# Kernel optimization log

Hardware: AMD Instinct MI355X
Metric: run time of the kernel (lower is better)

## Reference

```python
import jax, jax.numpy as jnp
import numpy as np

N = 100000          # nodes
E = 1600000         # edges (before self-loops)
F_IN = 256          # num_node_features
F_MID = F_IN // 2   # conv1 out = 128
HID = 128           # hidden_channels
OUT = 64            # num_label_features
G = 128             # num graphs in batch
NEG_SLOPE = 0.2


def setup_inputs() -> dict:
    key = jax.random.key(0)
    ks = jax.random.split(key, 16)
    s = 0.05
    return {
        "x": jax.random.normal(ks[0], (N, F_IN), dtype=jnp.float32),
        "edge_index": jax.random.randint(ks[1], (2, E), 0, N, dtype=jnp.int64),
        "batch": jnp.sort(jax.random.randint(ks[2], (N,), 0, G, dtype=jnp.int64)),
        # GATConv 1 (heads=1)
        "W1": jax.random.normal(ks[3], (F_IN, F_MID), jnp.float32) * s,
        "a1_src": jax.random.normal(ks[4], (F_MID,), jnp.float32) * s,
        "a1_dst": jax.random.normal(ks[5], (F_MID,), jnp.float32) * s,
        "b1": jnp.zeros((F_MID,), jnp.float32),
        # GATConv 2
        "W2": jax.random.normal(ks[6], (F_MID, HID), jnp.float32) * s,
        "a2_src": jax.random.normal(ks[7], (HID,), jnp.float32) * s,
        "a2_dst": jax.random.normal(ks[8], (HID,), jnp.float32) * s,
        "b2": jnp.zeros((HID,), jnp.float32),
        # GlobalAttention gate nn
        "gate_W": jax.random.normal(ks[9], (HID, 1), jnp.float32) * s,
        "gate_b": jnp.zeros((1,), jnp.float32),
        # final linear
        "lin_W": jax.random.normal(ks[10], (HID, OUT), jnp.float32) * s,
        "lin_b": jnp.zeros((OUT,), jnp.float32),
    }


def _gat_conv(x, edge_index, W, a_src, a_dst, bias):
    """PyG GATConv, heads=1, add_self_loops=True, negative_slope=0.2."""
    n = x.shape[0]
    h = x @ W                                   # [N, F]
    loop = jnp.arange(n, dtype=edge_index.dtype)
    src = jnp.concatenate([edge_index[0], loop])  # message sources j
    dst = jnp.concatenate([edge_index[1], loop])  # aggregation targets i
    # per-node attention logits, gathered per-edge
    al = (h @ a_src)[src] + (h @ a_dst)[dst]    # [E+N]
    al = jax.nn.leaky_relu(al, NEG_SLOPE)
    # segment softmax over incoming edges of each dst node
    m = jax.ops.segment_max(al, dst, num_segments=n)
    e = jnp.exp(al - m[dst])
    s = jax.ops.segment_sum(e, dst, num_segments=n)
    coef = e / (s[dst] + 1e-16)
    out = jax.ops.segment_sum(h[src] * coef[:, None], dst, num_segments=n)
    return out + bias


def reference(x, edge_index, batch, W1, a1_src, a1_dst, b1,
              W2, a2_src, a2_dst, b2, gate_W, gate_b, lin_W, lin_b):
    h = _gat_conv(x, edge_index, W1, a1_src, a1_dst, b1)
    h = jax.nn.relu(h)
    h = _gat_conv(h, edge_index, W2, a2_src, a2_dst, b2)
    # GlobalAttention pooling: segment softmax of gate over batch ids
    gate = (h @ gate_W + gate_b)[:, 0]          # [N]
    gm = jax.ops.segment_max(gate, batch, num_segments=G)
    ge = jnp.exp(gate - gm[batch])
    gs = jax.ops.segment_sum(ge, batch, num_segments=G)
    attn = ge / (gs[batch] + 1e-16)
    pooled = jax.ops.segment_sum(h * attn[:, None], batch, num_segments=G)  # [G, HID]
    pooled = jax.nn.relu(pooled)
    # dropout p=0.5 is identity at inference
    return pooled @ lin_W + lin_b               # [G, OUT]
```

## Files before the change

kernel.cpp:

```cpp
#include <hip/hip_runtime.h>
#include <hip/hip_bf16.h>
#include <math.h>

#define NNODES 100000
#define NEDGES 1600000
#define EN     1700000
#define F_IN   256
#define F_MID  128
#define HID    128
#define NG     128
#define NOUT   64
#define SCAN_CHUNK 2048
#define NCHUNK ((NNODES + SCAN_CHUNK - 1) / SCAN_CHUNK)

typedef unsigned int  u32;
typedef unsigned short u16;

__device__ __forceinline__ float bfl(u32 u) { return __uint_as_float(u << 16); }
__device__ __forceinline__ float bfh(u32 u) { return __uint_as_float(u & 0xFFFF0000u); }
__device__ __forceinline__ u32 f2bf(float f) {
    u32 x = __float_as_uint(f);
    return (x + 0x7FFFu + ((x >> 16) & 1u)) >> 16;
}

__global__ __launch_bounds__(256) void k_init(int* deg, float* gs, float* pooled) {
    int i = blockIdx.x * 256 + threadIdx.x;
    if (i < NNODES) deg[i] = 1;
    if (i < NG) gs[i] = 0.f;
    if (i < NG * HID) pooled[i] = 0.f;
}

__global__ __launch_bounds__(256) void k_count(const int* __restrict__ ei, int* deg) {
    int e = blockIdx.x * 256 + threadIdx.x;
    if (e >= NEDGES) return;
    atomicAdd(&deg[ei[NEDGES + e]], 1);
}

__global__ __launch_bounds__(256) void k_scan_chunk(const int* __restrict__ deg,
                                                    int* rowptr, int* part) {
    __shared__ int sums[256];
    int c = blockIdx.x, t = threadIdx.x;
    int base = c * SCAN_CHUNK;
    int v[8]; int s = 0;
#pragma unroll
    for (int i = 0; i < 8; i++) {
        int idx = base + t * 8 + i;
        v[i] = (idx < NNODES) ? deg[idx] : 0;
        s += v[i];
    }
    sums[t] = s;
    __syncthreads();
    for (int off = 1; off < 256; off <<= 1) {
        int x = (t >= off) ? sums[t - off] : 0;
        __syncthreads();
        sums[t] += x;
        __syncthreads();
    }
    int run = (t == 0) ? 0 : sums[t - 1];
#pragma unroll
    for (int i = 0; i < 8; i++) {
        int idx = base + t * 8 + i;
        if (idx < NNODES) rowptr[idx] = run;
        run += v[i];
    }
    if (t == 255) part[c] = sums[255];
}

__global__ void k_scan_part(int* part, int nc) {
    if (threadIdx.x == 0) {
        int run = 0;
        for (int c = 0; c < nc; c++) { int v = part[c]; part[c] = run; run += v; }
    }
}

__global__ __launch_bounds__(256) void k_scan_add(int* rowptr, int* cursor,
                                                  const int* __restrict__ part) {
    int i = blockIdx.x * 256 + threadIdx.x;
    if (i >= NNODES) return;
    int v = rowptr[i] + part[i >> 11];
    rowptr[i] = v;
    cursor[i] = v;
}

__global__ __launch_bounds__(256) void k_fill(const int* __restrict__ ei,
                                              int* cursor, int* srcs, int* dsts) {
    int e = blockIdx.x * 256 + threadIdx.x;
    if (e >= EN) return;
    int src, dst;
    if (e < NEDGES) { src = ei[e]; dst = ei[NEDGES + e]; }
    else            { src = dst = e - NEDGES; }
    int pos = atomicAdd(&cursor[dst], 1);
    srcs[pos] = src;
    dsts[pos] = dst;
}

__global__ __launch_bounds__(256) void k_coef(const int* __restrict__ srcs,
                                              const int* __restrict__ dsts,
                                              const float* __restrict__ as_,
                                              const float* __restrict__ ad_,
                                              int2* __restrict__ meta) {
    int e = blockIdx.x * 256 + threadIdx.x;
    if (e >= EN) return;
    int s = srcs[e], d = dsts[e];
    float al = as_[s] + ad_[d];
    al = (al > 0.f) ? al : 0.2f * al;
    float ev = __expf(al);
    meta[e] = make_int2(s, __float_as_int(ev));
}

template <int K, bool ABF>
__global__ __launch_bounds__(256) void k_gemm(const void* __restrict__ Av,
                                              const float* __restrict__ B,
                                              u16* __restrict__ C, int M) {
    __shared__ float As[16][128];
    __shared__ float Bs[16][128];
    int bm = blockIdx.x * 128;
    int tid = threadIdx.x;
    int tx = tid & 15, ty = tid >> 4;
    float acc[8][8] = {};
    for (int k0 = 0; k0 < K; k0 += 16) {
#pragma unroll
        for (int q = tid; q < 512; q += 256) {
            int m = q >> 2, kq = (q & 3) << 2;
            int row = bm + m;
            if (ABF) {
                const u16* A = (const u16*)Av;
                uint2 v = make_uint2(0u, 0u);
                if (row < M) v = *(const uint2*)(A + (size_t)row * K + k0 + kq);
                As[kq + 0][m] = bfl(v.x); As[kq + 1][m] = bfh(v.x);
                As[kq + 2][m] = bfl(v.y); As[kq + 3][m] = bfh(v.y);
            } else {
                const float* A = (const float*)Av;
                float4 v = make_float4(0.f, 0.f, 0.f, 0.f);
                if (row < M) v = *(const float4*)(A + (size_t)row * K + k0 + kq);
                As[kq + 0][m] = v.x; As[kq + 1][m] = v.y;
                As[kq + 2][m] = v.z; As[kq + 3][m] = v.w;
            }
        }
#pragma unroll
        for (int q = tid; q < 512; q += 256) {
            int kk = q >> 5, n4 = (q & 31) << 2;
            *(float4*)(&Bs[kk][n4]) = *(const float4*)(B + (size_t)(k0 + kk) * 128 + n4);
        }
        __syncthreads();
#pragma unroll
        for (int kk = 0; kk < 16; kk++) {
            float a[8], b[8];
            *(float4*)(a)     = *(float4*)(&As[kk][ty * 8]);
            *(float4*)(a + 4) = *(float4*)(&As[kk][ty * 8 + 4]);
            *(float4*)(b)     = *(float4*)(&Bs[kk][tx * 8]);
            *(float4*)(b + 4) = *(float4*)(&Bs[kk][tx * 8 + 4]);
#pragma unroll
            for (int i = 0; i < 8; i++)
#pragma unroll
                for (int j = 0; j < 8; j++)
                    acc[i][j] = fmaf(a[i], b[j], acc[i][j]);
        }
        __syncthreads();
    }
#pragma unroll
    for (int i = 0; i < 8; i++) {
        int row = bm + ty * 8 + i;
        if (row < M) {
            uint4 o;
            o.x = f2bf(acc[i][0]) | (f2bf(acc[i][1]) << 16);
            o.y = f2bf(acc[i][2]) | (f2bf(acc[i][3]) << 16);
            o.z = f2bf(acc[i][4]) | (f2bf(acc[i][5]) << 16);
            o.w = f2bf(acc[i][6]) | (f2bf(acc[i][7]) << 16);
            *(uint4*)(C + (size_t)row * 128 + tx * 8) = o;
        }
    }
}

__global__ __launch_bounds__(256) void k_dots(const u32* __restrict__ h,
                                              const float* __restrict__ asrc,
                                              const float* __restrict__ adst,
                                              float* as_, float* ad_) {
    int wid = (blockIdx.x * 256 + threadIdx.x) >> 6;
    int lane = threadIdx.x & 63;
    if (wid >= NNODES) return;
    u32 u = h[(size_t)wid * 64 + lane];
    float vx = bfl(u), vy = bfh(u);
    float2 as2 = ((const float2*)asrc)[lane];
    float2 ad2 = ((const float2*)adst)[lane];
    float s = vx * as2.x + vy * as2.y;
    float d = vx * ad2.x + vy * ad2.y;
#pragma unroll
    for (int off = 32; off; off >>= 1) {
        s += __shfl_xor(s, off);
        d += __shfl_xor(d, off);
    }
    if (lane == 0) { as_[wid] = s; ad_[wid] = d; }
}

template <bool RELU, bool GATE, bool OUTBF>
__global__ __launch_bounds__(256, 4) void k_agg(
    const u32* __restrict__ h, const int2* __restrict__ meta,
    const int* __restrict__ rowptr, const int* __restrict__ rowend,
    const float* __restrict__ bias, void* __restrict__ outv,
    const float* __restrict__ gateW, const float* __restrict__ gateB,
    float* __restrict__ gatev, float* __restrict__ gs,
    const int* __restrict__ batch) {
    int wid = (blockIdx.x * 256 + threadIdx.x) >> 6;
    int lane = threadIdx.x & 63;
    if (wid >= NNODES) return;
    int row = rowptr[wid];
    int dg = rowend[wid] - row;
    const int2* mp = meta + row;

    float ssum = 0.f;
    float2 a0 = {0.f, 0.f}, a1 = {0.f, 0.f}, a2 = {0.f, 0.f}, a3 = {0.f, 0.f};

    int i = 0;
    for (; i + 8 <= dg; i += 8) {
        int4 ma = *(const int4*)(mp + i);
        int4 mb = *(const int4*)(mp + i + 2);
        int4 mc = *(const int4*)(mp + i + 4);
        int4 md = *(const int4*)(mp + i + 6);
        u32 u0 = h[(size_t)ma.x * 64 + lane];
        u32 u1 = h[(size_t)ma.z * 64 + lane];
        u32 u2 = h[(size_t)mb.x * 64 + lane];
        u32 u3 = h[(size_t)mb.z * 64 + lane];
        u32 u4 = h[(size_t)mc.x * 64 + lane];
        u32 u5 = h[(size_t)mc.z * 64 + lane];
        u32 u6 = h[(size_t)md.x * 64 + lane];
        u32 u7 = h[(size_t)md.z * 64 + lane];
        float e0 = __int_as_float(ma.y), e1 = __int_as_float(ma.w);
        float e2 = __int_as_float(mb.y), e3 = __int_as_float(mb.w);
        float e4 = __int_as_float(mc.y), e5 = __int_as_float(mc.w);
        float e6 = __int_as_float(md.y), e7 = __int_as_float(md.w);
        ssum += ((e0 + e1) + (e2 + e3)) + ((e4 + e5) + (e6 + e7));
        a0.x = fmaf(e0, bfl(u0), a0.x); a0.y = fmaf(e0, bfh(u0), a0.y);
        a1.x = fmaf(e1, bfl(u1), a1.x); a1.y = fmaf(e1, bfh(u1), a1.y);
        a2.x = fmaf(e2, bfl(u2), a2.x); a2.y = fmaf(e2, bfh(u2), a2.y);
        a3.x = fmaf(e3, bfl(u3), a3.x); a3.y = fmaf(e3, bfh(u3), a3.y);
        a0.x = fmaf(e4, bfl(u4), a0.x); a0.y = fmaf(e4, bfh(u4), a0.y);
        a1.x = fmaf(e5, bfl(u5), a1.x); a1.y = fmaf(e5, bfh(u5), a1.y);
        a2.x = fmaf(e6, bfl(u6), a2.x); a2.y = fmaf(e6, bfh(u6), a2.y);
        a3.x = fmaf(e7, bfl(u7), a3.x); a3.y = fmaf(e7, bfh(u7), a3.y);
    }
    if (i + 4 <= dg) {
        int4 ma = *(const int4*)(mp + i);
        int4 mb = *(const int4*)(mp + i + 2);
        u32 u0 = h[(size_t)ma.x * 64 + lane];
        u32 u1 = h[(size_t)ma.z * 64 + lane];
        u32 u2 = h[(size_t)mb.x * 64 + lane];
        u32 u3 = h[(size_t)mb.z * 64 + lane];
        float e0 = __int_as_float(ma.y), e1 = __int_as_float(ma.w);
        float e2 = __int_as_float(mb.y), e3 = __int_as_float(mb.w);
        ssum += (e0 + e1) + (e2 + e3);
        a0.x = fmaf(e0, bfl(u0), a0.x); a0.y = fmaf(e0, bfh(u0), a0.y);
        a1.x = fmaf(e1, bfl(u1), a1.x); a1.y = fmaf(e1, bfh(u1), a1.y);
        a2.x = fmaf(e2, bfl(u2), a2.x); a2.y = fmaf(e2, bfh(u2), a2.y);
        a3.x = fmaf(e3, bfl(u3), a3.x); a3.y = fmaf(e3, bfh(u3), a3.y);
        i += 4;
    }
    if (i + 2 <= dg) {
        int4 ma = *(const int4*)(mp + i);
        u32 u0 = h[(size_t)ma.x * 64 + lane];
        u32 u1 = h[(size_t)ma.z * 64 + lane];
        float e0 = __int_as_float(ma.y), e1 = __int_as_float(ma.w);
        ssum += e0 + e1;
        a0.x = fmaf(e0, bfl(u0), a0.x); a0.y = fmaf(e0, bfh(u0), a0.y);
        a1.x = fmaf(e1, bfl(u1), a1.x); a1.y = fmaf(e1, bfh(u1), a1.y);
        i += 2;
    }
    if (i < dg) {
        int2 m = mp[i];
        u32 u0 = h[(size_t)m.x * 64 + lane];
        float e0 = __int_as_float(m.y);
        ssum += e0;
        a0.x = fmaf(e0, bfl(u0), a0.x); a0.y = fmaf(e0, bfh(u0), a0.y);
    }

    float2 acc;
    acc.x = (a0.x + a1.x) + (a2.x + a3.x);
    acc.y = (a0.y + a1.y) + (a2.y + a3.y);
    float inv = 1.f / (ssum + 1e-16f);
    float2 b2v = ((const float2*)bias)[lane];
    float o0 = acc.x * inv + b2v.x;
    float o1 = acc.y * inv + b2v.y;
    if (RELU) { o0 = fmaxf(o0, 0.f); o1 = fmaxf(o1, 0.f); }
    if (OUTBF) {
        ((u32*)outv)[(size_t)wid * 64 + lane] = f2bf(o0) | (f2bf(o1) << 16);
    } else {
        ((float2*)((float*)outv + (size_t)wid * 128))[lane] = make_float2(o0, o1);
    }
    if (GATE) {
        float2 gw = ((const float2*)gateW)[lane];
        float g = o0 * gw.x + o1 * gw.y;
#pragma unroll
        for (int off = 32; off; off >>= 1) g += __shfl_xor(g, off);
        if (lane == 0) {
            float ge = __expf(g + gateB[0]);
            gatev[wid] = ge;
            atomicAdd(&gs[batch[wid]], ge);
        }
    }
}

__global__ __launch_bounds__(128) void k_pool(const float* __restrict__ h,
                                              const float* __restrict__ gatev,
                                              const float* __restrict__ gs,
                                              const int* __restrict__ batch,
                                              float* pooled) {
    int t = threadIdx.x;
    int chunk = (NNODES + gridDim.x - 1) / gridDim.x;
    int s0 = blockIdx.x * chunk;
    int s1 = s0 + chunk; if (s1 > NNODES) s1 = NNODES;
    if (s0 >= s1) return;
    int curg = batch[s0];
    float invs = 1.f / (gs[curg] + 1e-16f);
    float acc = 0.f;
    for (int i = s0; i < s1; i++) {
        int g = batch[i];
        if (g != curg) {
            atomicAdd(&pooled[curg * 128 + t], acc);
            acc = 0.f; curg = g;
            invs = 1.f / (gs[g] + 1e-16f);
        }
        acc += h[(size_t)i * 128 + t] * (gatev[i] * invs);
    }
    atomicAdd(&pooled[curg * 128 + t], acc);
}

__global__ __launch_bounds__(64) void k_final(const float* __restrict__ pooled,
                                              const float* __restrict__ linW,
                                              const float* __restrict__ linb,
                                              float* __restrict__ out) {
    __shared__ float rowv[128];
    int g = blockIdx.x, t = threadIdx.x;
    rowv[t]      = fmaxf(pooled[g * 128 + t], 0.f);
    rowv[t + 64] = fmaxf(pooled[g * 128 + 64 + t], 0.f);
    __syncthreads();
    float acc = linb[t];
#pragma unroll 8
    for (int k = 0; k < 128; k++) acc = fmaf(rowv[k], linW[k * 64 + t], acc);
    out[g * 64 + t] = acc;
}

extern "C" void kernel_launch(void* const* d_in, const int* in_sizes, int n_in,
                              void* d_out, int out_size, void* d_ws, size_t ws_size,
                              hipStream_t stream) {
    const float* x     = (const float*)d_in[0];
    const int*   ei    = (const int*)d_in[1];
    const int*   batch = (const int*)d_in[2];
    const float* W1    = (const float*)d_in[3];
    const float* a1s   = (const float*)d_in[4];
    const float* a1d   = (const float*)d_in[5];
    const float* b1    = (const float*)d_in[6];
    const float* W2    = (const float*)d_in[7];
    const float* a2s   = (const float*)d_in[8];
    const float* a2d   = (const float*)d_in[9];
    const float* b2    = (const float*)d_in[10];
    const float* gateW = (const float*)d_in[11];
    const float* gateB = (const float*)d_in[12];
    const float* linW  = (const float*)d_in[13];
    const float* linb  = (const float*)d_in[14];
    float* out = (float*)d_out;

    char* p = (char*)d_ws;
    auto alloc = [&](size_t bytes) -> void* {
        void* r = (void*)p;
        p += (bytes + 255) & ~(size_t)255;
        return r;
    };
    u16*   hb     = (u16*)alloc((size_t)NNODES * 128 * 2);
    u16*   h1a    = (u16*)alloc((size_t)NNODES * 128 * 2);
    float* bufF   = (float*)alloc((size_t)NNODES * 128 * 4);
    float* as_    = (float*)alloc((size_t)NNODES * 4);
    float* ad_    = (float*)alloc((size_t)NNODES * 4);
    float* gatev  = (float*)alloc((size_t)NNODES * 4);
    int*   deg    = (int*)alloc((size_t)NNODES * 4);
    int*   rowptr = (int*)alloc((size_t)NNODES * 4);
    int*   cursor = (int*)alloc((size_t)NNODES * 4);
    int*   srcs   = (int*)alloc((size_t)EN * 4);
    int*   dsts   = (int*)alloc((size_t)EN * 4);
    int2*  meta   = (int2*)alloc((size_t)EN * 8);
    int*   part   = (int*)alloc(64 * 4);
    float* gs     = (float*)alloc(NG * 4);
    float* pooled = (float*)alloc((size_t)NG * HID * 4);

    const int gN   = (NNODES + 255) / 256;
    const int gE   = (NEDGES + 255) / 256;
    const int gEN  = (EN + 255) / 256;
    const int gW   = (NNODES + 3) / 4;

    k_init<<<gN, 256, 0, stream>>>(deg, gs, pooled);
    k_count<<<gE, 256, 0, stream>>>(ei, deg);
    k_scan_chunk<<<NCHUNK, 256, 0, stream>>>(deg, rowptr, part);
    k_scan_part<<<1, 64, 0, stream>>>(part, NCHUNK);
    k_scan_add<<<gN, 256, 0, stream>>>(rowptr, cursor, part);
    k_fill<<<gEN, 256, 0, stream>>>(ei, cursor, srcs, dsts);

    k_gemm<256, false><<<(NNODES + 127) / 128, 256, 0, stream>>>(x, W1, hb, NNODES);
    k_dots<<<gW, 256, 0, stream>>>((const u32*)hb, a1s, a1d, as_, ad_);
    k_coef<<<gEN, 256, 0, stream>>>(srcs, dsts, as_, ad_, meta);
    k_agg<true, false, true><<<gW, 256, 0, stream>>>((const u32*)hb, meta,
                                                     rowptr, cursor, b1, h1a,
                                                     nullptr, nullptr, nullptr,
                                                     nullptr, nullptr);
    k_gemm<128, true><<<(NNODES + 127) / 128, 256, 0, stream>>>(h1a, W2, hb, NNODES);
    k_dots<<<gW, 256, 0, stream>>>((const u32*)hb, a2s, a2d, as_, ad_);
    k_coef<<<gEN, 256, 0, stream>>>(srcs, dsts, as_, ad_, meta);
    k_agg<false, true, false><<<gW, 256, 0, stream>>>((const u32*)hb, meta,
                                                      rowptr, cursor, b2, bufF,
                                                      gateW, gateB, gatev, gs, batch);
    k_pool<<<512, 128, 0, stream>>>(bufF, gatev, gs, batch, pooled);
    k_final<<<NG, 64, 0, stream>>>(pooled, linW, linb, out);
}
```

Before: 1.222 ms.

## Switch GAT aggregation from dst-pull gather to src-push atomic scatter

Edges are now bucketed by source node instead of destination. Each wavefront loads its own node's feature row once and scatters e*h into a zeroed fp32 accumulator with float atomics. Softmax denominators are accumulated atomically in the coefficient kernel, and a separate normalise kernel applies the division, bias, ReLU, bf16 packing and gate. This removes the random feature-row gathers but adds about 128 atomic adds per edge, an extra 51MB fp32 accumulator round trip, and zeroing passes. The float output buffer now reuses the bf16 feature buffer region.

After: 2.564 ms. 110% more time.

```diff
diff --git a/kernel.cpp b/kernel.cpp
--- a/kernel.cpp
+++ b/kernel.cpp
@@ -33,7 +33,7 @@
 __global__ __launch_bounds__(256) void k_count(const int* __restrict__ ei, int* deg) {
     int e = blockIdx.x * 256 + threadIdx.x;
     if (e >= NEDGES) return;
-    atomicAdd(&deg[ei[NEDGES + e]], 1);
+    atomicAdd(&deg[ei[e]], 1);
 }
 
 __global__ __launch_bounds__(256) void k_scan_chunk(const int* __restrict__ deg,
@@ -89,23 +89,31 @@
     int src, dst;
     if (e < NEDGES) { src = ei[e]; dst = ei[NEDGES + e]; }
     else            { src = dst = e - NEDGES; }
-    int pos = atomicAdd(&cursor[dst], 1);
+    int pos = atomicAdd(&cursor[src], 1);
     srcs[pos] = src;
     dsts[pos] = dst;
+}
+
+__global__ __launch_bounds__(256) void k_zero(float4* acc4, float* ssum) {
+    int i = blockIdx.x * 256 + threadIdx.x;
+    acc4[i] = make_float4(0.f, 0.f, 0.f, 0.f);
+    if (i < NNODES) ssum[i] = 0.f;
 }
 
 __global__ __launch_bounds__(256) void k_coef(const int* __restrict__ srcs,
                                               const int* __restrict__ dsts,
                                               const float* __restrict__ as_,
                                               const float* __restrict__ ad_,
-                                              int2* __restrict__ meta) {
+                                              int2* __restrict__ meta,
+                                              float* __restrict__ ssum) {
     int e = blockIdx.x * 256 + threadIdx.x;
     if (e >= EN) return;
     int s = srcs[e], d = dsts[e];
     float al = as_[s] + ad_[d];
     al = (al > 0.f) ? al : 0.2f * al;
     float ev = __expf(al);
-    meta[e] = make_int2(s, __float_as_int(ev));
+    meta[e] = make_int2(d, __float_as_int(ev));
+    atomicAdd(&ssum[d], ev);
 }
 
 template <int K, bool ABF>
@@ -193,10 +201,46 @@
     if (lane == 0) { as_[wid] = s; ad_[wid] = d; }
 }
 
-template <bool RELU, bool GATE, bool OUTBF>
-__global__ __launch_bounds__(256, 4) void k_agg(
+__global__ __launch_bounds__(256) void k_scatter(
     const u32* __restrict__ h, const int2* __restrict__ meta,
     const int* __restrict__ rowptr, const int* __restrict__ rowend,
+    float* __restrict__ acc) {
+    int wid = (blockIdx.x * 256 + threadIdx.x) >> 6;
+    int lane = threadIdx.x & 63;
+    if (wid >= NNODES) return;
+    int row = rowptr[wid];
+    int end = rowend[wid];
+    u32 wlo = h[(size_t)wid * 64 + (lane >> 1)];
+    u32 whi = h[(size_t)wid * 64 + 32 + (lane >> 1)];
+    float hx = (lane & 1) ? bfh(wlo) : bfl(wlo);
+    float hy = (lane & 1) ? bfh(whi) : bfl(whi);
+    int e = row;
+    for (; e + 4 <= end; e += 4) {
+        int4 m01 = *(const int4*)(meta + e);
+        int4 m23 = *(const int4*)(meta + e + 2);
+        float e0 = __int_as_float(m01.y), e1 = __int_as_float(m01.w);
+        float e2 = __int_as_float(m23.y), e3 = __int_as_float(m23.w);
+        float* b0 = acc + (size_t)m01.x * 128;
+        float* b1 = acc + (size_t)m01.z * 128;
+        float* b2 = acc + (size_t)m23.x * 128;
+        float* b3 = acc + (size_t)m23.z * 128;
+        atomicAdd(b0 + lane, e0 * hx);      atomicAdd(b0 + 64 + lane, e0 * hy);
+        atomicAdd(b1 + lane, e1 * hx);      atomicAdd(b1 + 64 + lane, e1 * hy);
+        atomicAdd(b2 + lane, e2 * hx);      atomicAdd(b2 + 64 + lane, e2 * hy);
+        atomicAdd(b3 + lane, e3 * hx);      atomicAdd(b3 + 64 + lane, e3 * hy);
+    }
+    for (; e < end; e++) {
+        int2 m = meta[e];
+        float ev = __int_as_float(m.y);
+        float* b = acc + (size_t)m.x * 128;
+        atomicAdd(b + lane, ev * hx);
+        atomicAdd(b + 64 + lane, ev * hy);
+    }
+}
+
+template <bool RELU, bool OUTBF, bool GATE>
+__global__ __launch_bounds__(256) void k_norm(
+    const float* __restrict__ acc, const float* __restrict__ ssum,
     const float* __restrict__ bias, void* __restrict__ outv,
     const float* __restrict__ gateW, const float* __restrict__ gateB,
     float* __restrict__ gatev, float* __restrict__ gs,
@@ -204,91 +248,24 @@
     int wid = (blockIdx.x * 256 + threadIdx.x) >> 6;
     int lane = threadIdx.x & 63;
     if (wid >= NNODES) return;
-    int row = rowptr[wid];
-    int dg = rowend[wid] - row;
-    const int2* mp = meta + row;
-
-    float ssum = 0.f;
-    float2 a0 = {0.f, 0.f}, a1 = {0.f, 0.f}, a2 = {0.f, 0.f}, a3 = {0.f, 0.f};
-
-    int i = 0;
-    for (; i + 8 <= dg; i += 8) {
-        int4 ma = *(const int4*)(mp + i);
-        int4 mb = *(const int4*)(mp + i + 2);
-        int4 mc = *(const int4*)(mp + i + 4);
-        int4 md = *(const int4*)(mp + i + 6);
-        u32 u0 = h[(size_t)ma.x * 64 + lane];
-        u32 u1 = h[(size_t)ma.z * 64 + lane];
-        u32 u2 = h[(size_t)mb.x * 64 + lane];
-        u32 u3 = h[(size_t)mb.z * 64 + lane];
-        u32 u4 = h[(size_t)mc.x * 64 + lane];
-        u32 u5 = h[(size_t)mc.z * 64 + lane];
-        u32 u6 = h[(size_t)md.x * 64 + lane];
-        u32 u7 = h[(size_t)md.z * 64 + lane];
-        float e0 = __int_as_float(ma.y), e1 = __int_as_float(ma.w);
-        float e2 = __int_as_float(mb.y), e3 = __int_as_float(mb.w);
-        float e4 = __int_as_float(mc.y), e5 = __int_as_float(mc.w);
-        float e6 = __int_as_float(md.y), e7 = __int_as_float(md.w);
-        ssum += ((e0 + e1) + (e2 + e3)) + ((e4 + e5) + (e6 + e7));
-        a0.x = fmaf(e0, bfl(u0), a0.x); a0.y = fmaf(e0, bfh(u0), a0.y);
-        a1.x = fmaf(e1, bfl(u1), a1.x); a1.y = fmaf(e1, bfh(u1), a1.y);
-        a2.x = fmaf(e2, bfl(u2), a2.x); a2.y = fmaf(e2, bfh(u2), a2.y);
-        a3.x = fmaf(e3, bfl(u3), a3.x); a3.y = fmaf(e3, bfh(u3), a3.y);
-        a0.x = fmaf(e4, bfl(u4), a0.x); a0.y = fmaf(e4, bfh(u4), a0.y);
-        a1.x = fmaf(e5, bfl(u5), a1.x); a1.y = fmaf(e5, bfh(u5), a1.y);
-        a2.x = fmaf(e6, bfl(u6), a2.x); a2.y = fmaf(e6, bfh(u6), a2.y);
-        a3.x = fmaf(e7, bfl(u7), a3.x); a3.y = fmaf(e7, bfh(u7), a3.y);
-    }
-    if (i + 4 <= dg) {
-        int4 ma = *(const int4*)(mp + i);
-        int4 mb = *(const int4*)(mp + i + 2);
-        u32 u0 = h[(size_t)ma.x * 64 + lane];
-        u32 u1 = h[(size_t)ma.z * 64 + lane];
-        u32 u2 = h[(size_t)mb.x * 64 + lane];
-        u32 u3 = h[(size_t)mb.z * 64 + lane];
-        float e0 = __int_as_float(ma.y), e1 = __int_as_float(ma.w);
-        float e2 = __int_as_float(mb.y), e3 = __int_as_float(mb.w);
-        ssum += (e0 + e1) + (e2 + e3);
-        a0.x = fmaf(e0, bfl(u0), a0.x); a0.y = fmaf(e0, bfh(u0), a0.y);
-        a1.x = fmaf(e1, bfl(u1), a1.x); a1.y = fmaf(e1, bfh(u1), a1.y);
-        a2.x = fmaf(e2, bfl(u2), a2.x); a2.y = fmaf(e2, bfh(u2), a2.y);
-        a3.x = fmaf(e3, bfl(u3), a3.x); a3.y = fmaf(e3, bfh(u3), a3.y);
-        i += 4;
-    }
-    if (i + 2 <= dg) {
-        int4 ma = *(const int4*)(mp + i);
-        u32 u0 = h[(size_t)ma.x * 64 + lane];
-        u32 u1 = h[(size_t)ma.z * 64 + lane];
-        float e0 = __int_as_float(ma.y), e1 = __int_as_float(ma.w);
-        ssum += e0 + e1;
-        a0.x = fmaf(e0, bfl(u0), a0.x); a0.y = fmaf(e0, bfh(u0), a0.y);
-        a1.x = fmaf(e1, bfl(u1), a1.x); a1.y = fmaf(e1, bfh(u1), a1.y);
-        i += 2;
-    }
-    if (i < dg) {
-        int2 m = mp[i];
-        u32 u0 = h[(size_t)m.x * 64 + lane];
-        float e0 = __int_as_float(m.y);
-        ssum += e0;
-        a0.x = fmaf(e0, bfl(u0), a0.x); a0.y = fmaf(e0, bfh(u0), a0.y);
-    }
-
-    float2 acc;
-    acc.x = (a0.x + a1.x) + (a2.x + a3.x);
-    acc.y = (a0.y + a1.y) + (a2.y + a3.y);
-    float inv = 1.f / (ssum + 1e-16f);
-    float2 b2v = ((const float2*)bias)[lane];
-    float o0 = acc.x * inv + b2v.x;
-    float o1 = acc.y * inv + b2v.y;
+    float inv = 1.f / (ssum[wid] + 1e-16f);
+    float o0 = acc[(size_t)wid * 128 + lane] * inv + bias[lane];
+    float o1 = acc[(size_t)wid * 128 + 64 + lane] * inv + bias[lane + 64];
     if (RELU) { o0 = fmaxf(o0, 0.f); o1 = fmaxf(o1, 0.f); }
     if (OUTBF) {
-        ((u32*)outv)[(size_t)wid * 64 + lane] = f2bf(o0) | (f2bf(o1) << 16);
+        int w2  = (2 * lane) & 63, w2b = (2 * lane + 1) & 63;
+        float t0 = __shfl(o0, w2),  t1 = __shfl(o1, w2);
+        float s0 = __shfl(o0, w2b), s1 = __shfl(o1, w2b);
+        float flo = (lane < 32) ? t0 : t1;
+        float fhi = (lane < 32) ? s0 : s1;
+        ((u32*)outv)[(size_t)wid * 64 + lane] = f2bf(flo) | (f2bf(fhi) << 16);
     } else {
-        ((float2*)((float*)outv + (size_t)wid * 128))[lane] = make_float2(o0, o1);
+        float* o = (float*)outv;
+        o[(size_t)wid * 128 + lane] = o0;
+        o[(size_t)wid * 128 + 64 + lane] = o1;
     }
     if (GATE) {
-        float2 gw = ((const float2*)gateW)[lane];
-        float g = o0 * gw.x + o1 * gw.y;
+        float g = o0 * gateW[lane] + o1 * gateW[lane + 64];
 #pragma unroll
         for (int off = 32; off; off >>= 1) g += __shfl_xor(g, off);
         if (lane == 0) {
@@ -367,10 +344,12 @@
     };
     u16*   hb     = (u16*)alloc((size_t)NNODES * 128 * 2);
     u16*   h1a    = (u16*)alloc((size_t)NNODES * 128 * 2);
-    float* bufF   = (float*)alloc((size_t)NNODES * 128 * 4);
+    float* bufF   = (float*)hb;
+    float* acc    = (float*)alloc((size_t)NNODES * 128 * 4);
     float* as_    = (float*)alloc((size_t)NNODES * 4);
     float* ad_    = (float*)alloc((size_t)NNODES * 4);
     float* gatev  = (float*)alloc((size_t)NNODES * 4);
+    float* ssum   = (float*)alloc((size_t)NNODES * 4);
     int*   deg    = (int*)alloc((size_t)NNODES * 4);
     int*   rowptr = (int*)alloc((size_t)NNODES * 4);
     int*   cursor = (int*)alloc((size_t)NNODES * 4);
@@ -385,6 +364,7 @@
     const int gE   = (NEDGES + 255) / 256;
     const int gEN  = (EN + 255) / 256;
     const int gW   = (NNODES + 3) / 4;
+    const int gZ   = (NNODES * 32 + 255) / 256;
 
     k_init<<<gN, 256, 0, stream>>>(deg, gs, pooled);
     k_count<<<gE, 256, 0, stream>>>(ei, deg);
@@ -395,17 +375,19 @@
 
     k_gemm<256, false><<<(NNODES + 127) / 128, 256, 0, stream>>>(x, W1, hb, NNODES);
     k_dots<<<gW, 256, 0, stream>>>((const u32*)hb, a1s, a1d, as_, ad_);
-    k_coef<<<gEN, 256, 0, stream>>>(srcs, dsts, as_, ad_, meta);
-    k_agg<true, false, true><<<gW, 256, 0, stream>>>((const u32*)hb, meta,
-                                                     rowptr, cursor, b1, h1a,
-                                                     nullptr, nullptr, nullptr,
-                                                     nullptr, nullptr);
+    k_zero<<<gZ, 256, 0, stream>>>((float4*)acc, ssum);
+    k_coef<<<gEN, 256, 0, stream>>>(srcs, dsts, as_, ad_, meta, ssum);
+    k_scatter<<<gW, 256, 0, stream>>>((const u32*)hb, meta, rowptr, cursor, acc);
+    k_norm<true, true, false><<<gW, 256, 0, stream>>>(acc, ssum, b1, h1a,
+                                                      nullptr, nullptr, nullptr,
+                                                      nullptr, nullptr);
     k_gemm<128, true><<<(NNODES + 127) / 128, 256, 0, stream>>>(h1a, W2, hb, NNODES);
     k_dots<<<gW, 256, 0, stream>>>((const u32*)hb, a2s, a2d, as_, ad_);
-    k_coef<<<gEN, 256, 0, stream>>>(srcs, dsts, as_, ad_, meta);
-    k_agg<false, true, false><<<gW, 256, 0, stream>>>((const u32*)hb, meta,
-                                                      rowptr, cursor, b2, bufF,
-                                                      gateW, gateB, gatev, gs, batch);
+    k_zero<<<gZ, 256, 0, stream>>>((float4*)acc, ssum);
+    k_coef<<<gEN, 256, 0, stream>>>(srcs, dsts, as_, ad_, meta, ssum);
+    k_scatter<<<gW, 256, 0, stream>>>((const u32*)hb, meta, rowptr, cursor, acc);
+    k_norm<false, false, true><<<gW, 256, 0, stream>>>(acc, ssum, b2, bufF,
+                                                       gateW, gateB, gatev, gs, batch);
     k_pool<<<512, 128, 0, stream>>>(bufF, gatev, gs, batch, pooled);
     k_final<<<NG, 64, 0, stream>>>(pooled, linW, linb, out);
 }
```
